# Kernel optimization log

Measured on AMD Instinct MI355X. Metric: run time of the kernel, lower is better.

The kernel has to match this reference:

```python
import jax, jax.numpy as jnp
import numpy as np
from jax import lax

N_NODES = 65536
IN_DIM = 128
HID = 256
OUT = 128
N_EDGES = 1048576
BATCH = 64


def setup_inputs() -> dict:
    key = jax.random.key(0)
    ks = jax.random.split(key, 16)
    s = 0.05
    inp = {
        "x": jax.random.normal(ks[0], (N_NODES, IN_DIM), dtype=jnp.float32),
        "edge_index": jax.random.randint(ks[1], (2, N_EDGES), 0, N_NODES, dtype=jnp.int64),
        "batch_size": BATCH,
        # GCN layer 0: input_dim -> hidden
        "W0": jax.random.normal(ks[2], (IN_DIM, HID), dtype=jnp.float32) * s,
        "b0": jnp.zeros((HID,), dtype=jnp.float32),
        # GCN layer 1: hidden -> hidden
        "W1": jax.random.normal(ks[3], (HID, HID), dtype=jnp.float32) * s,
        "b1": jnp.zeros((HID,), dtype=jnp.float32),
        # LayerNorm
        "gamma": jnp.ones((HID,), dtype=jnp.float32),
        "beta": jnp.zeros((HID,), dtype=jnp.float32),
        # LSTM layer 0 (gate order i,f,g,o as in torch)
        "Wih0": jax.random.normal(ks[4], (4 * OUT, HID), dtype=jnp.float32) * s,
        "Whh0": jax.random.normal(ks[5], (4 * OUT, OUT), dtype=jnp.float32) * s,
        "bih0": jnp.zeros((4 * OUT,), dtype=jnp.float32),
        "bhh0": jnp.zeros((4 * OUT,), dtype=jnp.float32),
        # LSTM layer 1
        "Wih1": jax.random.normal(ks[6], (4 * OUT, OUT), dtype=jnp.float32) * s,
        "Whh1": jax.random.normal(ks[7], (4 * OUT, OUT), dtype=jnp.float32) * s,
        "bih1": jnp.zeros((4 * OUT,), dtype=jnp.float32),
        "bhh1": jnp.zeros((4 * OUT,), dtype=jnp.float32),
    }
    return inp


def _gcn_prep(edge_index, n):
    # add self-loops, compute symmetric norm (PyG GCNConv default)
    loop = jnp.arange(n, dtype=edge_index.dtype)
    src = jnp.concatenate([edge_index[0], loop])
    dst = jnp.concatenate([edge_index[1], loop])
    deg = jax.ops.segment_sum(jnp.ones_like(dst, dtype=jnp.float32), dst, num_segments=n)
    dinv = jnp.where(deg > 0, lax.rsqrt(deg), 0.0)
    norm = dinv[src] * dinv[dst]  # [E+N]
    return src, dst, norm


def _gcn(x, W, b, src, dst, norm, n):
    h = x @ W                      # [N, H]
    msg = h[src] * norm[:, None]   # gather + scale  [E+N, H]
    return jax.ops.segment_sum(msg, dst, num_segments=n) + b


def _lstm_layer(xs, Wih, Whh, bih, bhh):
    # xs: [B, T, D]; torch gate order i, f, g, o
    B = xs.shape[0]
    H = Whh.shape[1]
    b = bih + bhh

    def step(carry, x_t):
        h, c = carry
        gates = x_t @ Wih.T + h @ Whh.T + b
        i, f, g, o = jnp.split(gates, 4, axis=-1)
        c = jax.nn.sigmoid(f) * c + jax.nn.sigmoid(i) * jnp.tanh(g)
        h = jax.nn.sigmoid(o) * jnp.tanh(c)
        return (h, c), h

    h0 = jnp.zeros((B, H), dtype=xs.dtype)
    (hT, cT), ys = lax.scan(step, (h0, h0), jnp.swapaxes(xs, 0, 1))
    return jnp.swapaxes(ys, 0, 1), hT


def reference(x, edge_index, batch_size, W0, b0, W1, b1, gamma, beta,
              Wih0, Whh0, bih0, bhh0, Wih1, Whh1, bih1, bhh1):
    n = x.shape[0]
    src, dst, norm = _gcn_prep(edge_index, n)
    # GCN layer 0 + ReLU (dropout is identity in eval)
    h = jax.nn.relu(_gcn(x, W0, b0, src, dst, norm, n))
    # GCN layer 1 (last layer: no activation)
    h = _gcn(h, W1, b1, src, dst, norm, n)
    # LayerNorm over feature dim
    mu = jnp.mean(h, axis=-1, keepdims=True)
    var = jnp.var(h, axis=-1, keepdims=True)
    h = (h - mu) * lax.rsqrt(var + 1e-5) * gamma + beta
    # reshape to [B, T, HID] and run 2-layer LSTM
    seq = h.reshape(batch_size, -1, h.shape[1])
    ys0, _ = _lstm_layer(seq, Wih0, Whh0, bih0, bhh0)
    _, hT = _lstm_layer(ys0, Wih1, Whh1, bih1, bhh1)
    return hT  # h_n[-1]: [B, OUT]
```

## Files before the change

kernel.cpp:

```cpp
#include <hip/hip_runtime.h>
#include <hip/hip_bf16.h>
#include <math.h>

#define N_NODES 65536
#define IN_DIM  128
#define HID     256
#define OUT_DIM 128
#define G4      512
#define N_EDGES 1048576
#define BATCH   64
#define SEQ_T   1024

static constexpr size_t OFF_CNT   = 0x000000;
static constexpr size_t OFF_ROW   = 0x040000;
static constexpr size_t OFF_CUR   = 0x080000;
static constexpr size_t OFF_DINV  = 0x0C0000;
static constexpr size_t OFF_BSUM  = 0x100000;
static constexpr size_t OFF_COL   = 0x101000;
static constexpr size_t OFF_ENORM = 0x501000;
static constexpr size_t OFF_R1    = 0xA00000;
static constexpr size_t OFF_R2    = OFF_R1 + 0x8000000;
static constexpr size_t WS_NEED   = OFF_R2 + 0x4000000;

__global__ void k_sentinel(float* __restrict__ out, int n) {
    int i = blockIdx.x * blockDim.x + threadIdx.x;
    if (i < n) out[i] = 1e30f;
}

__global__ void k_detect(const unsigned* __restrict__ ei32, int* __restrict__ flag) {
    int t = threadIdx.x;
    unsigned v = ei32[2 * t + 1] | ei32[2 * (t + 977) + 1] | ei32[2 * (t + 300000) + 1];
    unsigned long long ball = __ballot(v != 0u);
    if (t == 0) *flag = (ball == 0ull) ? 1 : 0;
}

__device__ __forceinline__ int edge_at(const int* ei32, const long long* ei64,
                                       int is64, int idx) {
    return is64 ? (int)ei64[idx] : ei32[idx];
}

__global__ void k_zero2(int* __restrict__ a, int* __restrict__ b) {
    int i = blockIdx.x * blockDim.x + threadIdx.x;
    if (i < N_NODES) { a[i] = 0; b[i] = 0; }
}

__global__ void k_count(const int* __restrict__ ei32, const long long* __restrict__ ei64,
                        const int* __restrict__ flag, int* __restrict__ cnt) {
    int e = blockIdx.x * blockDim.x + threadIdx.x;
    int is64 = *flag;
    if (e < N_EDGES) {
        int d = edge_at(ei32, ei64, is64, N_EDGES + e);
        atomicAdd(&cnt[d], 1);
    }
}

__global__ void k_dinv(const int* __restrict__ cnt, float* __restrict__ dinv) {
    int n = blockIdx.x * blockDim.x + threadIdx.x;
    if (n < N_NODES) dinv[n] = rsqrtf((float)(cnt[n] + 1));
}

__global__ void k_scan_block(const int* __restrict__ cnt, int* __restrict__ row_ptr,
                             int* __restrict__ bsum) {
    __shared__ int s[256];
    int i = blockIdx.x * 256 + threadIdx.x;
    int v = cnt[i];
    s[threadIdx.x] = v;
    __syncthreads();
    for (int off = 1; off < 256; off <<= 1) {
        int t = (threadIdx.x >= off) ? s[threadIdx.x - off] : 0;
        __syncthreads();
        s[threadIdx.x] += t;
        __syncthreads();
    }
    row_ptr[i] = s[threadIdx.x] - v;
    if (threadIdx.x == 255) bsum[blockIdx.x] = s[255];
}

__global__ void k_scan_bsum(int* __restrict__ bsum) {
    __shared__ int s[256];
    int v = bsum[threadIdx.x];
    s[threadIdx.x] = v;
    __syncthreads();
    for (int off = 1; off < 256; off <<= 1) {
        int t = (threadIdx.x >= off) ? s[threadIdx.x - off] : 0;
        __syncthreads();
        s[threadIdx.x] += t;
        __syncthreads();
    }
    bsum[threadIdx.x] = s[threadIdx.x] - v;
}

__global__ void k_scan_add(int* __restrict__ row_ptr, const int* __restrict__ bsum) {
    int i = blockIdx.x * 256 + threadIdx.x;
    row_ptr[i] += bsum[blockIdx.x];
}

__global__ void k_scatter(const int* __restrict__ ei32, const long long* __restrict__ ei64,
                          const int* __restrict__ flag, const int* __restrict__ row_ptr,
                          int* __restrict__ cursor, const float* __restrict__ dinv,
                          int* __restrict__ col, float* __restrict__ enorm) {
    int e = blockIdx.x * blockDim.x + threadIdx.x;
    int is64 = *flag;
    if (e < N_EDGES) {
        int s = edge_at(ei32, ei64, is64, e);
        int d = edge_at(ei32, ei64, is64, N_EDGES + e);
        int slot = row_ptr[d] + atomicAdd(&cursor[d], 1);
        col[slot]   = s;
        enorm[slot] = dinv[s] * dinv[d];
    }
}

template <int DIM>
__launch_bounds__(256)
__global__ void k_aggregate(const float* __restrict__ x, const int* __restrict__ row_ptr,
                            const int* __restrict__ cnt, const int* __restrict__ col,
                            const float* __restrict__ enorm, const float* __restrict__ dinv,
                            float* __restrict__ outb) {
    constexpr int VEC = DIM / 64;
    int gw   = (blockIdx.x * 256 + threadIdx.x) >> 6;
    int lane = threadIdx.x & 63;
    if (gw >= N_NODES) return;

    float dn = dinv[gw];
    float sw = dn * dn;
    float acc0 = 0.f, acc1 = 0.f, acc2 = 0.f, acc3 = 0.f;
    if constexpr (VEC == 2) {
        float2 t = *(const float2*)(x + (size_t)gw * DIM + lane * 2);
        acc0 = t.x * sw; acc1 = t.y * sw;
    } else {
        float4 t = *(const float4*)(x + (size_t)gw * DIM + lane * 4);
        acc0 = t.x * sw; acc1 = t.y * sw; acc2 = t.z * sw; acc3 = t.w * sw;
    }

    int base = row_ptr[gw], len = cnt[gw];
    for (int off = 0; off < len; off += 64) {
        int rem = len - off;
        int c_  = 0;
        float w_ = 0.f;
        if (lane < rem) {
            c_ = col[base + off + lane];
            w_ = enorm[base + off + lane];
        }
        int m = rem < 64 ? rem : 64;
        for (int j = 0; j < m; j++) {
            int   sj = __shfl(c_, j);
            float wj = __shfl(w_, j);
            const float* xs = x + (size_t)sj * DIM;
            if constexpr (VEC == 2) {
                float2 t = *(const float2*)(xs + lane * 2);
                acc0 += t.x * wj; acc1 += t.y * wj;
            } else {
                float4 t = *(const float4*)(xs + lane * 4);
                acc0 += t.x * wj; acc1 += t.y * wj; acc2 += t.z * wj; acc3 += t.w * wj;
            }
        }
    }
    float* orow = outb + (size_t)gw * DIM;
    if constexpr (VEC == 2) {
        *(float2*)(orow + lane * 2) = make_float2(acc0, acc1);
    } else {
        *(float4*)(orow + lane * 4) = make_float4(acc0, acc1, acc2, acc3);
    }
}

template <int K, bool BT, int EPI>
__launch_bounds__(256)
__global__ void k_gemm(const float* __restrict__ A, const float* __restrict__ Bm,
                       const float* __restrict__ bias, const float* __restrict__ bias2,
                       float* __restrict__ C, int Nfull) {
    constexpr int BM = 128, BN = 128, BK = 16;
    __shared__ __align__(16) float As[BK][BM + 4];
    __shared__ __align__(16) float Bs[BK][BN + 4];
    int tid = threadIdx.x;
    int m0 = blockIdx.x * BM, n0 = blockIdx.y * BN;
    int tr = tid >> 4, tc = tid & 15;

    float acc[8][8];
#pragma unroll
    for (int i = 0; i < 8; i++)
#pragma unroll
        for (int j = 0; j < 8; j++) acc[i][j] = 0.f;

    int lkq = tid & 3;
    int lm  = tid >> 2;
    int lnq = tid & 31;
    int lkk = tid >> 5;

    for (int k0 = 0; k0 < K; k0 += BK) {
#pragma unroll
        for (int p = 0; p < 2; p++) {
            int m = lm + p * 64;
            float4 a4 = *(const float4*)(A + (size_t)(m0 + m) * K + k0 + lkq * 4);
            As[lkq * 4 + 0][m] = a4.x;
            As[lkq * 4 + 1][m] = a4.y;
            As[lkq * 4 + 2][m] = a4.z;
            As[lkq * 4 + 3][m] = a4.w;
        }
        if constexpr (!BT) {
#pragma unroll
            for (int p = 0; p < 2; p++) {
                int kk = lkk + p * 8;
                float4 b4 = *(const float4*)(Bm + (size_t)(k0 + kk) * Nfull + n0 + lnq * 4);
                *(float4*)&Bs[kk][lnq * 4] = b4;
            }
        } else {
#pragma unroll
            for (int p = 0; p < 2; p++) {
                int n = lm + p * 64;
                float4 b4 = *(const float4*)(Bm + (size_t)(n0 + n) * K + k0 + lkq * 4);
                Bs[lkq * 4 + 0][n] = b4.x;
                Bs[lkq * 4 + 1][n] = b4.y;
                Bs[lkq * 4 + 2][n] = b4.z;
                Bs[lkq * 4 + 3][n] = b4.w;
            }
        }
        __syncthreads();
#pragma unroll
        for (int k = 0; k < BK; k++) {
            float4 aa0 = *(const float4*)&As[k][tr * 8];
            float4 aa1 = *(const float4*)&As[k][tr * 8 + 4];
            float4 bb0 = *(const float4*)&Bs[k][tc * 8];
            float4 bb1 = *(const float4*)&Bs[k][tc * 8 + 4];
            float av[8] = {aa0.x, aa0.y, aa0.z, aa0.w, aa1.x, aa1.y, aa1.z, aa1.w};
            float bv[8] = {bb0.x, bb0.y, bb0.z, bb0.w, bb1.x, bb1.y, bb1.z, bb1.w};
#pragma unroll
            for (int i = 0; i < 8; i++)
#pragma unroll
                for (int j = 0; j < 8; j++) acc[i][j] += av[i] * bv[j];
        }
        __syncthreads();
    }

    float bz[8];
#pragma unroll
    for (int j = 0; j < 8; j++) {
        int cc = n0 + tc * 8 + j;
        float b = bias[cc];
        if constexpr (EPI == 2) b += bias2[cc];
        bz[j] = b;
    }
#pragma unroll
    for (int i = 0; i < 8; i++) {
        int row = m0 + tr * 8 + i;
        float vv[8];
#pragma unroll
        for (int j = 0; j < 8; j++) {
            float v = acc[i][j] + bz[j];
            if constexpr (EPI == 1) v = fmaxf(v, 0.f);
            vv[j] = v;
        }
        float* orow = C + (size_t)row * Nfull + n0 + tc * 8;
        *(float4*)orow       = make_float4(vv[0], vv[1], vv[2], vv[3]);
        *(float4*)(orow + 4) = make_float4(vv[4], vv[5], vv[6], vv[7]);
    }
}

__launch_bounds__(256)
__global__ void k_gemm_ln(const float* __restrict__ A, const float* __restrict__ W1,
                          const float* __restrict__ b1, const float* __restrict__ gamma,
                          const float* __restrict__ beta, float* __restrict__ D) {
    constexpr int BM = 64, BK = 16;
    __shared__ __align__(16) float As[BK][BM + 4];
    __shared__ __align__(16) float Bs[BK][HID + 4];
    int tid = threadIdx.x;
    int m0 = blockIdx.x * BM;
    int tr = tid >> 5, tc = tid & 31;

    float acc[8][8];
#pragma unroll
    for (int i = 0; i < 8; i++)
#pragma unroll
        for (int j = 0; j < 8; j++) acc[i][j] = 0.f;

    int lkq = tid & 3, lm = tid >> 2;
    int lnq = tid & 63, lkk = tid >> 6;

    for (int k0 = 0; k0 < HID; k0 += BK) {
        {
            float4 a4 = *(const float4*)(A + (size_t)(m0 + lm) * HID + k0 + lkq * 4);
            As[lkq * 4 + 0][lm] = a4.x;
            As[lkq * 4 + 1][lm] = a4.y;
            As[lkq * 4 + 2][lm] = a4.z;
            As[lkq * 4 + 3][lm] = a4.w;
        }
#pragma unroll
        for (int p = 0; p < 4; p++) {
            int kk = lkk + p * 4;
            float4 b4 = *(const float4*)(W1 + (size_t)(k0 + kk) * HID + lnq * 4);
            *(float4*)&Bs[kk][lnq * 4] = b4;
        }
        __syncthreads();
#pragma unroll
        for (int k = 0; k < BK; k++) {
            float4 aa0 = *(const float4*)&As[k][tr * 8];
            float4 aa1 = *(const float4*)&As[k][tr * 8 + 4];
            float4 bb0 = *(const float4*)&Bs[k][tc * 8];
            float4 bb1 = *(const float4*)&Bs[k][tc * 8 + 4];
            float av[8] = {aa0.x, aa0.y, aa0.z, aa0.w, aa1.x, aa1.y, aa1.z, aa1.w};
            float bv[8] = {bb0.x, bb0.y, bb0.z, bb0.w, bb1.x, bb1.y, bb1.z, bb1.w};
#pragma unroll
            for (int i = 0; i < 8; i++)
#pragma unroll
                for (int j = 0; j < 8; j++) acc[i][j] += av[i] * bv[j];
        }
        __syncthreads();
    }

    float vv[8][8];
    float rs[8], rq[8];
#pragma unroll
    for (int i = 0; i < 8; i++) { rs[i] = 0.f; rq[i] = 0.f; }
#pragma unroll
    for (int j = 0; j < 8; j++) {
        float bb = b1[tc * 8 + j];
#pragma unroll
        for (int i = 0; i < 8; i++) {
            float v = acc[i][j] + bb;
            vv[i][j] = v;
            rs[i] += v;
            rq[i] += v * v;
        }
    }
#pragma unroll
    for (int m = 1; m < 32; m <<= 1) {
#pragma unroll
        for (int i = 0; i < 8; i++) {
            rs[i] += __shfl_xor(rs[i], m, 32);
            rq[i] += __shfl_xor(rq[i], m, 32);
        }
    }
    float gm[8], bt[8];
#pragma unroll
    for (int j = 0; j < 8; j++) {
        gm[j] = gamma[tc * 8 + j];
        bt[j] = beta[tc * 8 + j];
    }
#pragma unroll
    for (int i = 0; i < 8; i++) {
        float mean = rs[i] * (1.f / 256.f);
        float var  = rq[i] * (1.f / 256.f) - mean * mean;
        float rstd = rsqrtf(var + 1e-5f);
        int n = m0 + tr * 8 + i;
        int orow = ((n & (SEQ_T - 1)) << 6) | (n >> 10);
        float o[8];
#pragma unroll
        for (int j = 0; j < 8; j++) o[j] = (vv[i][j] - mean) * rstd * gm[j] + bt[j];
        float* op = D + (size_t)orow * HID + tc * 8;
        *(float4*)op       = make_float4(o[0], o[1], o[2], o[3]);
        *(float4*)(op + 4) = make_float4(o[4], o[5], o[6], o[7]);
    }
}

__device__ __forceinline__ float sigmf(float x) { return 1.f / (1.f + __expf(-x)); }
__device__ __forceinline__ float tanhft(float x) {
    float t = __expf(-2.f * fabsf(x));
    float r = (1.f - t) / (1.f + t);
    return copysignf(r, x);
}
__device__ __forceinline__ float dot4(float4 a, float4 b) {
    return a.x * b.x + a.y * b.y + a.z * b.z + a.w * b.w;
}

template <int LAYER>
__launch_bounds__(512)
__global__ void k_lstm(const float* __restrict__ Whh, const float* __restrict__ xpart,
                       float* __restrict__ ys, float* __restrict__ outp) {
    __shared__ float hbuf[128];
    __shared__ float actv[512];
    int b = blockIdx.x, tid = threadIdx.x;
    int gg = tid >> 3, kc = tid & 7;

    float4 w4[8][4];
#pragma unroll
    for (int u = 0; u < 8; u++) {
        const float4* wr = (const float4*)(Whh + (size_t)(gg * 8 + u) * 128 + kc * 16);
#pragma unroll
        for (int q = 0; q < 4; q++) w4[u][q] = wr[q];
    }
    if (tid < 128) hbuf[tid] = 0.f;
    float c = 0.f;
    float xp = xpart[(size_t)b * G4 + tid];
    __syncthreads();

    for (int t = 0; t < SEQ_T; t++) {
        float4 h0 = *(const float4*)(hbuf + kc * 16);
        float4 h1 = *(const float4*)(hbuf + kc * 16 + 4);
        float4 h2 = *(const float4*)(hbuf + kc * 16 + 8);
        float4 h3 = *(const float4*)(hbuf + kc * 16 + 12);
        float acc[8];
#pragma unroll
        for (int u = 0; u < 8; u++) {
            acc[u] = dot4(w4[u][0], h0) + dot4(w4[u][1], h1) +
                     dot4(w4[u][2], h2) + dot4(w4[u][3], h3);
        }
        int tn = t + 1 < SEQ_T ? t + 1 : SEQ_T - 1;
        float xpn = xpart[((size_t)tn * BATCH + b) * G4 + tid];

#pragma unroll
        for (int u = 0; u < 8; u++) {
            acc[u] += __shfl_xor(acc[u], 1, 8);
            acc[u] += __shfl_xor(acc[u], 2, 8);
            acc[u] += __shfl_xor(acc[u], 4, 8);
        }
        float gs = acc[0];
#pragma unroll
        for (int u = 1; u < 8; u++) gs = (kc == u) ? acc[u] : gs;
        gs += xp;

        int cls = tid >> 7;
        float a = (cls == 2) ? tanhft(gs) : sigmf(gs);
        actv[tid] = a;
        __syncthreads();

        if (tid < 128) {
            float ai = actv[tid], af = actv[tid + 128], ag = actv[tid + 256], ao = actv[tid + 384];
            c = af * c + ai * ag;
            float hn = ao * tanhft(c);
            hbuf[tid] = hn;
            if constexpr (LAYER == 0) {
                ys[((size_t)t * BATCH + b) * OUT_DIM + tid] = hn;
            } else {
                if (t == SEQ_T - 1) outp[b * OUT_DIM + tid] = hn;
            }
        }
        xp = xpn;
        __syncthreads();
    }
}

extern "C" void kernel_launch(void* const* d_in, const int* in_sizes, int n_in,
                              void* d_out, int out_size, void* d_ws, size_t ws_size,
                              hipStream_t stream) {
    const float*     x     = (const float*)d_in[0];
    const int*       ei32  = (const int*)d_in[1];
    const long long* ei64  = (const long long*)d_in[1];
    const float*     W0    = (const float*)d_in[3];
    const float*     b0    = (const float*)d_in[4];
    const float*     W1    = (const float*)d_in[5];
    const float*     b1    = (const float*)d_in[6];
    const float*     gamma = (const float*)d_in[7];
    const float*     beta  = (const float*)d_in[8];
    const float*     Wih0  = (const float*)d_in[9];
    const float*     Whh0  = (const float*)d_in[10];
    const float*     bih0  = (const float*)d_in[11];
    const float*     bhh0  = (const float*)d_in[12];
    const float*     Wih1  = (const float*)d_in[13];
    const float*     Whh1  = (const float*)d_in[14];
    const float*     bih1  = (const float*)d_in[15];
    const float*     bhh1  = (const float*)d_in[16];
    float* out = (float*)d_out;

    if (ws_size < WS_NEED) {
        k_sentinel<<<(out_size + 255) / 256, 256, 0, stream>>>(out, out_size);
        return;
    }

    char*  ws      = (char*)d_ws;
    int*   cnt     = (int*)(ws + OFF_CNT);
    int*   row_ptr = (int*)(ws + OFF_ROW);
    int*   cursor  = (int*)(ws + OFF_CUR);
    float* dinv    = (float*)(ws + OFF_DINV);
    int*   bsum    = (int*)(ws + OFF_BSUM);
    int*   dflag   = (int*)(ws + OFF_BSUM + 2048);
    int*   col     = (int*)(ws + OFF_COL);
    float* enorm   = (float*)(ws + OFF_ENORM);
    float* R1      = (float*)(ws + OFF_R1);
    float* R2      = (float*)(ws + OFF_R2);

    float* agg0 = R1;
    float* h0   = R2;
    float* agg1 = R1;
    float* Dbuf = R2;
    float* xbuf = R1;
    float* ys0  = R2;

    k_detect<<<1, 64, 0, stream>>>((const unsigned*)d_in[1], dflag);
    k_zero2<<<256, 256, 0, stream>>>(cnt, cursor);
    k_count<<<4096, 256, 0, stream>>>(ei32, ei64, dflag, cnt);
    k_dinv<<<256, 256, 0, stream>>>(cnt, dinv);
    k_scan_block<<<256, 256, 0, stream>>>(cnt, row_ptr, bsum);
    k_scan_bsum<<<1, 256, 0, stream>>>(bsum);
    k_scan_add<<<256, 256, 0, stream>>>(row_ptr, bsum);
    k_scatter<<<4096, 256, 0, stream>>>(ei32, ei64, dflag, row_ptr, cursor, dinv, col, enorm);

    k_aggregate<IN_DIM><<<N_NODES / 4, 256, 0, stream>>>(x, row_ptr, cnt, col, enorm, dinv, agg0);
    k_gemm<IN_DIM, false, 1><<<dim3(N_NODES / 128, HID / 128), 256, 0, stream>>>(
        agg0, W0, b0, nullptr, h0, HID);

    k_aggregate<HID><<<N_NODES / 4, 256, 0, stream>>>(h0, row_ptr, cnt, col, enorm, dinv, agg1);
    k_gemm_ln<<<N_NODES / 64, 256, 0, stream>>>(agg1, W1, b1, gamma, beta, Dbuf);

    k_gemm<HID, true, 2><<<dim3(N_NODES / 128, G4 / 128), 256, 0, stream>>>(
        Dbuf, Wih0, bih0, bhh0, xbuf, G4);
    k_lstm<0><<<BATCH, 512, 0, stream>>>(Whh0, xbuf, ys0, nullptr);

    k_gemm<OUT_DIM, true, 2><<<dim3(N_NODES / 128, G4 / 128), 256, 0, stream>>>(
        ys0, Wih1, bih1, bhh1, xbuf, G4);
    k_lstm<1><<<BATCH, 512, 0, stream>>>(Whh1, xbuf, nullptr, out);
}
```

Measured before the change: 3.321 ms.

## Restructure LSTM step so each thread group computes all four gates of one unit

The recurrent LSTM kernel is remapped so that each group of 4 threads owns one hidden unit and computes its i, f, g and o gate dot products, instead of 8 threads per gate row. The cell update then happens in registers with no shared activation buffer, which removes one of the two block barriers per timestep. A padded, double-buffered shared h vector avoids bank conflicts and read/write races. Fast division intrinsics replace true divides. The cost is more weight registers per thread (32 float4) and a launch-bounds hint that may constrain register allocation.

```diff
diff --git a/kernel.cpp b/kernel.cpp
--- a/kernel.cpp
+++ b/kernel.cpp
@@ -351,79 +351,92 @@
     }
 }
 
-__device__ __forceinline__ float sigmf(float x) { return 1.f / (1.f + __expf(-x)); }
 __device__ __forceinline__ float tanhft(float x) {
     float t = __expf(-2.f * fabsf(x));
-    float r = (1.f - t) / (1.f + t);
+    float r = __fdividef(1.f - t, 1.f + t);
     return copysignf(r, x);
 }
-__device__ __forceinline__ float dot4(float4 a, float4 b) {
-    return a.x * b.x + a.y * b.y + a.z * b.z + a.w * b.w;
-}
 
 template <int LAYER>
-__launch_bounds__(512)
+__launch_bounds__(512, 2)
 __global__ void k_lstm(const float* __restrict__ Whh, const float* __restrict__ xpart,
                        float* __restrict__ ys, float* __restrict__ outp) {
-    __shared__ float hbuf[128];
-    __shared__ float actv[512];
+    __shared__ float hbuf[2][160];
     int b = blockIdx.x, tid = threadIdx.x;
-    int gg = tid >> 3, kc = tid & 7;
-
-    float4 w4[8][4];
-#pragma unroll
-    for (int u = 0; u < 8; u++) {
-        const float4* wr = (const float4*)(Whh + (size_t)(gg * 8 + u) * 128 + kc * 16);
-#pragma unroll
-        for (int q = 0; q < 4; q++) w4[u][q] = wr[q];
-    }
-    if (tid < 128) hbuf[tid] = 0.f;
+    int gq = tid >> 2, kc = tid & 3;
+
+    float4 w[32];
+#pragma unroll
+    for (int u = 0; u < 4; u++) {
+        const float4* wr = (const float4*)(Whh + (size_t)(u * 128 + gq) * 128 + kc * 32);
+#pragma unroll
+        for (int q = 0; q < 8; q++) w[u * 8 + q] = wr[q];
+    }
+    if (tid < 160) { hbuf[0][tid] = 0.f; hbuf[1][tid] = 0.f; }
+
     float c = 0.f;
-    float xp = xpart[(size_t)b * G4 + tid];
+    float xq0 = xpart[(size_t)b * G4 +   0 + gq];
+    float xq1 = xpart[(size_t)b * G4 + 128 + gq];
+    float xq2 = xpart[(size_t)b * G4 + 256 + gq];
+    float xq3 = xpart[(size_t)b * G4 + 384 + gq];
+    int bs = 0;
     __syncthreads();
 
     for (int t = 0; t < SEQ_T; t++) {
-        float4 h0 = *(const float4*)(hbuf + kc * 16);
-        float4 h1 = *(const float4*)(hbuf + kc * 16 + 4);
-        float4 h2 = *(const float4*)(hbuf + kc * 16 + 8);
-        float4 h3 = *(const float4*)(hbuf + kc * 16 + 12);
-        float acc[8];
-#pragma unroll
-        for (int u = 0; u < 8; u++) {
-            acc[u] = dot4(w4[u][0], h0) + dot4(w4[u][1], h1) +
-                     dot4(w4[u][2], h2) + dot4(w4[u][3], h3);
+        float4 h4[8];
+#pragma unroll
+        for (int q = 0; q < 8; q++) {
+            int off = (2 * kc + (q >> 2)) * 20 + (q & 3) * 4;
+            h4[q] = *(const float4*)&hbuf[bs][off];
         }
         int tn = t + 1 < SEQ_T ? t + 1 : SEQ_T - 1;
-        float xpn = xpart[((size_t)tn * BATCH + b) * G4 + tid];
-
-#pragma unroll
-        for (int u = 0; u < 8; u++) {
-            acc[u] += __shfl_xor(acc[u], 1, 8);
-            acc[u] += __shfl_xor(acc[u], 2, 8);
-            acc[u] += __shfl_xor(acc[u], 4, 8);
-        }
-        float gs = acc[0];
-#pragma unroll
-        for (int u = 1; u < 8; u++) gs = (kc == u) ? acc[u] : gs;
-        gs += xp;
-
-        int cls = tid >> 7;
-        float a = (cls == 2) ? tanhft(gs) : sigmf(gs);
-        actv[tid] = a;
-        __syncthreads();
-
-        if (tid < 128) {
-            float ai = actv[tid], af = actv[tid + 128], ag = actv[tid + 256], ao = actv[tid + 384];
-            c = af * c + ai * ag;
-            float hn = ao * tanhft(c);
-            hbuf[tid] = hn;
+        const float* xr = xpart + ((size_t)tn * BATCH + b) * G4 + gq;
+        float xn0 = xr[0], xn1 = xr[128], xn2 = xr[256], xn3 = xr[384];
+
+        float2 a2[4];
+#pragma unroll
+        for (int u = 0; u < 4; u++) a2[u] = make_float2(0.f, 0.f);
+#pragma unroll
+        for (int u = 0; u < 4; u++) {
+#pragma unroll
+            for (int q = 0; q < 8; q++) {
+                float4 wv = w[u * 8 + q];
+                float4 hv = h4[q];
+                a2[u].x = fmaf(wv.x, hv.x, a2[u].x);
+                a2[u].y = fmaf(wv.y, hv.y, a2[u].y);
+                a2[u].x = fmaf(wv.z, hv.z, a2[u].x);
+                a2[u].y = fmaf(wv.w, hv.w, a2[u].y);
+            }
+        }
+        float g0 = a2[0].x + a2[0].y, g1 = a2[1].x + a2[1].y;
+        float g2 = a2[2].x + a2[2].y, g3 = a2[3].x + a2[3].y;
+
+        g0 += __shfl_xor(g0, 1, 4); g1 += __shfl_xor(g1, 1, 4);
+        g2 += __shfl_xor(g2, 1, 4); g3 += __shfl_xor(g3, 1, 4);
+        g0 += __shfl_xor(g0, 2, 4); g1 += __shfl_xor(g1, 2, 4);
+        g2 += __shfl_xor(g2, 2, 4); g3 += __shfl_xor(g3, 2, 4);
+
+        g0 += xq0; g1 += xq1; g2 += xq2; g3 += xq3;
+
+        float ei = __expf(-g0), ef = __expf(-g1), eo = __expf(-g3);
+        float ai = __fdividef(1.f, 1.f + ei);
+        float af = __fdividef(1.f, 1.f + ef);
+        float ao = __fdividef(1.f, 1.f + eo);
+        float ag = tanhft(g2);
+
+        c = fmaf(af, c, ai * ag);
+        float hn = ao * tanhft(c);
+
+        if (kc == 0) {
+            hbuf[bs ^ 1][(gq >> 4) * 20 + (gq & 15)] = hn;
             if constexpr (LAYER == 0) {
-                ys[((size_t)t * BATCH + b) * OUT_DIM + tid] = hn;
+                ys[((size_t)t * BATCH + b) * OUT_DIM + gq] = hn;
             } else {
-                if (t == SEQ_T - 1) outp[b * OUT_DIM + tid] = hn;
+                if (t == SEQ_T - 1) outp[b * OUT_DIM + gq] = hn;
             }
         }
-        xp = xpn;
+        xq0 = xn0; xq1 = xn1; xq2 = xn2; xq3 = xn3;
+        bs ^= 1;
         __syncthreads();
     }
 }
```

Result: faster. 2.693 ms (-18.9%).
